# Performance work log

Hardware: AMD Instinct MI355X
Metric: run time of the kernel (lower is better)

The kernel has to match this reference:

```python
import jax, jax.numpy as jnp
import numpy as np

SCALE_FACTOR = 8.0  # sqrt(head_dim=64)
GAMMA = 1.0
NEG_INF = -1e9


def setup_inputs() -> dict:
    key = jax.random.key(0)
    kq, kk, kv, km = jax.random.split(key, 4)
    B, H, S, D = 4, 16, 2048, 64
    q = jax.random.normal(kq, (B, H, S, D), dtype=jnp.float32)
    k = jax.random.normal(kk, (B, H, S, D), dtype=jnp.float32)
    v = jax.random.normal(kv, (B, H, S, D), dtype=jnp.float32)
    mask = jax.random.randint(km, (B, 1, S, S), 0, 2, dtype=jnp.int32)
    return {"q": q, "k": k, "v": v, "mask": mask}


def reference(q, k, v, mask):
    # attn = (q/scale) @ k^T, masked, softmax along last dim, scaled by gamma
    scores = jnp.einsum("bhsd,bhtd->bhst", q / SCALE_FACTOR, k)  # [B,H,S,S]
    scores = jnp.where(mask == 0, NEG_INF, scores)
    attn = jax.nn.softmax(scores, axis=-1) * GAMMA
    output = jnp.einsum("bhst,bhtd->bhsd", attn, v) + v  # AV + residual V
    return (output, attn)
```

## Files before the change

kernel.cpp:

```cpp
#include <hip/hip_runtime.h>

typedef _Float16 f16;
typedef _Float16 f16x4 __attribute__((ext_vector_type(4)));
typedef _Float16 f16x8 __attribute__((ext_vector_type(8)));
typedef float f32x16 __attribute__((ext_vector_type(16)));

#define MFMA16(a, b, c) __builtin_amdgcn_mfma_f32_32x32x16_f16((a), (b), (c), 0, 0, 0)

constexpr int B_ = 4, H_ = 16, S_ = 2048, D_ = 64, BH = 64;
constexpr int QB = 128;
constexpr int WQ = 32;
constexpr int KB = 64;
constexpr int TS = 512;
constexpr int NSPLIT = S_ / TS;
constexpr int NKT_W = TS / KB;
constexpr int NKT = S_ / KB;
constexpr size_t OUT0 = (size_t)B_ * H_ * S_ * D_;

__device__ __forceinline__ int swzb(int row, int col ) {
  int byte = (row << 7) + (col << 1);
  return byte ^ ((row & 7) << 4);
}

__device__ __forceinline__ void kload256(const float* g, int kt, int tid, float4 kr[4]) {
#pragma unroll
  for (int rep = 0; rep < 4; ++rep) {
    int idx = (rep * 256 + tid) * 4;
    kr[rep] = *(const float4*)(g + (size_t)(kt * KB + (idx >> 6)) * D_ + (idx & 63));
  }
}
__device__ __forceinline__ void kwrite256(char* KlB, int tid, const float4 kr[4]) {
#pragma unroll
  for (int rep = 0; rep < 4; ++rep) {
    int idx = (rep * 256 + tid) * 4;
    f16x4 hx = {(f16)kr[rep].x, (f16)kr[rep].y, (f16)kr[rep].z, (f16)kr[rep].w};
    *(f16x4*)(KlB + swzb(idx >> 6, idx & 63)) = hx;
  }
}
__device__ __forceinline__ void vwrite256(char* VtB, int tid, const float4 vr[4]) {
#pragma unroll
  for (int rep = 0; rep < 4; ++rep) {
    int idx = (rep * 256 + tid) * 4;
    int row = idx >> 6, col = idx & 63;
    *(f16*)(VtB + swzb(col + 0, row)) = (f16)vr[rep].x;
    *(f16*)(VtB + swzb(col + 1, row)) = (f16)vr[rep].y;
    *(f16*)(VtB + swzb(col + 2, row)) = (f16)vr[rep].z;
    *(f16*)(VtB + swzb(col + 3, row)) = (f16)vr[rep].w;
  }
}

__device__ __forceinline__ void load_qf(const float* qg, int qrow, int hi, f16x8 qf[4]) {
  const float* qr = qg + (size_t)qrow * D_;
#pragma unroll
  for (int s = 0; s < 4; ++s) {
    const int d0 = s * 16 + hi * 8;
    float4 a = *(const float4*)(qr + d0);
    float4 c = *(const float4*)(qr + d0 + 4);
    f16x8 t;
    t[0] = (f16)(a.x * 0.125f); t[1] = (f16)(a.y * 0.125f);
    t[2] = (f16)(a.z * 0.125f); t[3] = (f16)(a.w * 0.125f);
    t[4] = (f16)(c.x * 0.125f); t[5] = (f16)(c.y * 0.125f);
    t[6] = (f16)(c.z * 0.125f); t[7] = (f16)(c.w * 0.125f);
    qf[s] = t;
  }
}

__device__ __forceinline__ f32x16 qk8(const char* KlB, const f16x8 qf[4], int sub, int ln, int hi) {
  f32x16 s;
#pragma unroll
  for (int i = 0; i < 16; ++i) s[i] = 0.0f;
#pragma unroll
  for (int t = 0; t < 4; ++t) {
    f16x8 kf = *(const f16x8*)(KlB + swzb(sub * 32 + ln, t * 16 + hi * 8));
    s = MFMA16(qf[t], kf, s);
  }
  return s;
}

__global__ void zero_ws(float* __restrict__ p, int n) {
  int i = blockIdx.x * blockDim.x + threadIdx.x;
  if (i < n) p[i] = 0.0f;
}

__global__ __launch_bounds__(256, 4) void attn_rsum(
    const float* __restrict__ qg_, const float* __restrict__ kg_,
    const int* __restrict__ mg_, float* __restrict__ ws) {
  __shared__ f16 Kl[KB * D_];
  const int tid = threadIdx.x, lane = tid & 63, wid = tid >> 6;
  const int ln = lane & 31, hi = lane >> 5;
  const int bh = blockIdx.z, b = bh >> 4;
  const int qb = blockIdx.x * QB + wid * WQ;
  const int kt0 = blockIdx.y * NKT_W;
  const float* qg = qg_ + (size_t)bh * S_ * D_;
  const float* kg = kg_ + (size_t)bh * S_ * D_;
  const int* mg = mg_ + (size_t)b * S_ * S_;
  char* KlB = (char*)Kl;

  f16x8 qf[4];
  load_qf(qg, qb + ln, hi, qf);
  float rs[16];
#pragma unroll
  for (int r = 0; r < 16; ++r) rs[r] = 0.0f;

  float4 kr[4];
  kload256(kg, kt0, tid, kr);
  for (int i = 0; i < NKT_W; ++i) {
    __syncthreads();
    kwrite256(KlB, tid, kr);
    if (i + 1 < NKT_W) kload256(kg, kt0 + i + 1, tid, kr);
    __syncthreads();
#pragma unroll
    for (int sub = 0; sub < 2; ++sub) {
      const int t0 = (kt0 + i) * KB + sub * 32;
      const int* mrow = mg + (size_t)(qb + 4 * hi) * S_ + t0 + ln;
      int mk[16];
#pragma unroll
      for (int r = 0; r < 16; ++r) {
        const int qoff = (r & 3) + 8 * (r >> 2);
        mk[r] = mrow[(size_t)qoff * S_];
      }
      f32x16 sacc = qk8(KlB, qf, sub, ln, hi);
#pragma unroll
      for (int r = 0; r < 16; ++r) rs[r] += mk[r] ? __expf(sacc[r]) : 0.0f;
    }
  }
  float* wsrow = ws + (size_t)bh * S_;
#pragma unroll
  for (int r = 0; r < 16; ++r) {
    float s = rs[r];
    s += __shfl_xor(s, 16); s += __shfl_xor(s, 8); s += __shfl_xor(s, 4);
    s += __shfl_xor(s, 2); s += __shfl_xor(s, 1);
    if (ln == 0) {
      const int qoff = (r & 3) + 8 * (r >> 2);
      atomicAdd(wsrow + qb + qoff + 4 * hi, s);
    }
  }
}

__global__ __launch_bounds__(256, 4) void attn_emit(
    const float* __restrict__ qg_, const float* __restrict__ kg_,
    const int* __restrict__ mg_, const float* __restrict__ ws,
    float* __restrict__ out) {
  __shared__ f16 Kl[KB * D_];
  const int tid = threadIdx.x, lane = tid & 63, wid = tid >> 6;
  const int ln = lane & 31, hi = lane >> 5;
  const int bh = blockIdx.z, b = bh >> 4;
  const int qb = blockIdx.x * QB + wid * WQ;
  const int kt0 = blockIdx.y * NKT_W;
  const float* qg = qg_ + (size_t)bh * S_ * D_;
  const float* kg = kg_ + (size_t)bh * S_ * D_;
  const int* mg = mg_ + (size_t)b * S_ * S_;
  float* attnp = out + OUT0 + (size_t)bh * S_ * S_;
  char* KlB = (char*)Kl;

  f16x8 qf[4];
  load_qf(qg, qb + ln, hi, qf);
  const float* wsrow = ws + (size_t)bh * S_;
  float rinv[16];
#pragma unroll
  for (int r = 0; r < 16; ++r) {
    const int qoff = (r & 3) + 8 * (r >> 2);
    rinv[r] = 1.0f / wsrow[qb + qoff + 4 * hi];
  }

  float4 kr[4];
  kload256(kg, kt0, tid, kr);
  for (int i = 0; i < NKT_W; ++i) {
    __syncthreads();
    kwrite256(KlB, tid, kr);
    if (i + 1 < NKT_W) kload256(kg, kt0 + i + 1, tid, kr);
    __syncthreads();
#pragma unroll
    for (int sub = 0; sub < 2; ++sub) {
      const int t0 = (kt0 + i) * KB + sub * 32;
      const int* mrow = mg + (size_t)(qb + 4 * hi) * S_ + t0 + ln;
      int mk[16];
#pragma unroll
      for (int r = 0; r < 16; ++r) {
        const int qoff = (r & 3) + 8 * (r >> 2);
        mk[r] = mrow[(size_t)qoff * S_];
      }
      f32x16 sacc = qk8(KlB, qf, sub, ln, hi);
      float* arow = attnp + (size_t)(qb + 4 * hi) * S_ + t0 + ln;
#pragma unroll
      for (int r = 0; r < 16; ++r) {
        const int qoff = (r & 3) + 8 * (r >> 2);
        float p = mk[r] ? __expf(sacc[r]) * rinv[r] : 0.0f;
        arow[(size_t)qoff * S_] = p;
      }
    }
  }
}

__global__ __launch_bounds__(256) void attn_out(
    const float* __restrict__ qg_, const float* __restrict__ kg_,
    const float* __restrict__ vg_, const int* __restrict__ mg_,
    const float* __restrict__ ws, float* __restrict__ out) {
  __shared__ f16 Kl[KB * D_];
  __shared__ f16 Vt[D_ * KB];
  __shared__ f16 Pl[4 * WQ * KB];
  const int tid = threadIdx.x, lane = tid & 63, wid = tid >> 6;
  const int ln = lane & 31, hi = lane >> 5;
  const int bh = blockIdx.y, b = bh >> 4;
  const int qb = blockIdx.x * QB + wid * WQ;
  const float* qg = qg_ + (size_t)bh * S_ * D_;
  const float* kg = kg_ + (size_t)bh * S_ * D_;
  const float* vg = vg_ + (size_t)bh * S_ * D_;
  const int* mg = mg_ + (size_t)b * S_ * S_;
  float* outp = out + (size_t)bh * S_ * D_;
  char* KlB = (char*)Kl;
  char* VtB = (char*)Vt;
  char* PlB = (char*)Pl + wid * (WQ * KB * 2);

  f16x8 qf[4];
  load_qf(qg, qb + ln, hi, qf);
  const float* wsrow = ws + (size_t)bh * S_;
  float rinv[16];
#pragma unroll
  for (int r = 0; r < 16; ++r) {
    const int qoff = (r & 3) + 8 * (r >> 2);
    rinv[r] = 1.0f / wsrow[qb + qoff + 4 * hi];
  }

  f32x16 oacc0, oacc1;
#pragma unroll
  for (int i = 0; i < 16; ++i) { oacc0[i] = 0.0f; oacc1[i] = 0.0f; }

  float4 kr[4], vr[4];
  kload256(kg, 0, tid, kr);
  kload256(vg, 0, tid, vr);
  for (int kt = 0; kt < NKT; ++kt) {
    __syncthreads();
    kwrite256(KlB, tid, kr);
    vwrite256(VtB, tid, vr);
    if (kt + 1 < NKT) {
      kload256(kg, kt + 1, tid, kr);
      kload256(vg, kt + 1, tid, vr);
    }
    __syncthreads();
#pragma unroll
    for (int sub = 0; sub < 2; ++sub) {
      const int t0 = kt * KB + sub * 32;
      const int* mrow = mg + (size_t)(qb + 4 * hi) * S_ + t0 + ln;
      int mk[16];
#pragma unroll
      for (int r = 0; r < 16; ++r) {
        const int qoff = (r & 3) + 8 * (r >> 2);
        mk[r] = mrow[(size_t)qoff * S_];
      }
      f32x16 sacc = qk8(KlB, qf, sub, ln, hi);
#pragma unroll
      for (int r = 0; r < 16; ++r) {
        const int qoff = (r & 3) + 8 * (r >> 2);
        float p = mk[r] ? __expf(sacc[r]) * rinv[r] : 0.0f;
        *(f16*)(PlB + swzb(qoff + 4 * hi, sub * 32 + ln)) = (f16)p;
      }
    }
#pragma unroll
    for (int ts = 0; ts < 4; ++ts) {
      f16x8 pa = *(const f16x8*)(PlB + swzb(ln, ts * 16 + hi * 8));
      f16x8 vb0 = *(const f16x8*)(VtB + swzb(ln, ts * 16 + hi * 8));
      f16x8 vb1 = *(const f16x8*)(VtB + swzb(32 + ln, ts * 16 + hi * 8));
      oacc0 = MFMA16(pa, vb0, oacc0);
      oacc1 = MFMA16(pa, vb1, oacc1);
    }
  }

#pragma unroll
  for (int r = 0; r < 16; ++r) {
    const int qoff = (r & 3) + 8 * (r >> 2);
    const size_t o = (size_t)(qb + qoff + 4 * hi) * D_ + ln;
    outp[o] = oacc0[r] + vg[o];
    outp[o + 32] = oacc1[r] + vg[o + 32];
  }
}

extern "C" void kernel_launch(void* const* d_in, const int* in_sizes, int n_in,
                              void* d_out, int out_size, void* d_ws, size_t ws_size,
                              hipStream_t stream) {
  (void)in_sizes; (void)n_in; (void)out_size; (void)ws_size;
  const float* q = (const float*)d_in[0];
  const float* k = (const float*)d_in[1];
  const float* v = (const float*)d_in[2];
  const int* mask = (const int*)d_in[3];
  float* out = (float*)d_out;
  float* wsf = (float*)d_ws;

  const int nsum = BH * S_;
  zero_ws<<<dim3((nsum + 255) / 256), dim3(256), 0, stream>>>(wsf, nsum);
  attn_rsum<<<dim3(S_ / QB, NSPLIT, BH), dim3(256), 0, stream>>>(q, k, mask, wsf);
  attn_emit<<<dim3(S_ / QB, NSPLIT, BH), dim3(256), 0, stream>>>(q, k, mask, wsf, out);
  attn_out<<<dim3(S_ / QB, BH), dim3(256), 0, stream>>>(q, k, v, mask, wsf, out);
}
```

Measured before the change: 2.154 ms.

## Pack int32 mask into bitmask and remap block order across XCDs

Adds a pre-pass that turns the int32 mask into a bitmask with one bit per element, using wavefront ballots. All three attention kernels then read one 32-bit word per row per 32 keys instead of 32 ints, cutting the mask traffic that each of the three passes repeats. The grids are also flattened to 1D and block indices remapped, (i&7)*N + (i>>3), so that consecutive work items land on the same XCD and share cache. The cost is an extra kernel launch and workspace for the packed mask.

```diff
diff --git a/kernel.cpp b/kernel.cpp
--- a/kernel.cpp
+++ b/kernel.cpp
@@ -15,7 +15,9 @@
 constexpr int NSPLIT = S_ / TS;
 constexpr int NKT_W = TS / KB;
 constexpr int NKT = S_ / KB;
+constexpr int MW = S_ / 32;
 constexpr size_t OUT0 = (size_t)B_ * H_ * S_ * D_;
+constexpr size_t WS_RSUM_OFF = (size_t)B_ * S_ * MW;
 
 __device__ __forceinline__ int swzb(int row, int col ) {
   int byte = (row << 7) + (col << 1);
@@ -82,18 +84,36 @@
   if (i < n) p[i] = 0.0f;
 }
 
+__global__ __launch_bounds__(256) void mask_pack(const int* __restrict__ mg,
+                                                 unsigned* __restrict__ mb) {
+  const int tid = threadIdx.x, lane = tid & 63, wid = tid >> 6;
+  const int row = blockIdx.x * 4 + wid;
+  const int* mrow = mg + (size_t)row * S_;
+  unsigned long long myw = 0;
+#pragma unroll
+  for (int w = 0; w < 32; ++w) {
+    int m = mrow[w * 64 + lane];
+    unsigned long long bal = __ballot(m != 0);
+    if (lane == w) myw = bal;
+  }
+  if (lane < 32) *(unsigned long long*)(mb + (size_t)row * MW + 2 * lane) = myw;
+}
+
 __global__ __launch_bounds__(256, 4) void attn_rsum(
     const float* __restrict__ qg_, const float* __restrict__ kg_,
-    const int* __restrict__ mg_, float* __restrict__ ws) {
+    const unsigned* __restrict__ mb, float* __restrict__ ws) {
   __shared__ f16 Kl[KB * D_];
   const int tid = threadIdx.x, lane = tid & 63, wid = tid >> 6;
   const int ln = lane & 31, hi = lane >> 5;
-  const int bh = blockIdx.z, b = bh >> 4;
-  const int qb = blockIdx.x * QB + wid * WQ;
-  const int kt0 = blockIdx.y * NKT_W;
+  const int i = blockIdx.x;
+  const int work = (i & 7) * 512 + (i >> 3);
+  const int bh = work >> 6, rem = work & 63;
+  const int qb = (rem & 15) * QB + wid * WQ;
+  const int kt0 = (rem >> 4) * NKT_W;
+  const int b = bh >> 4;
   const float* qg = qg_ + (size_t)bh * S_ * D_;
   const float* kg = kg_ + (size_t)bh * S_ * D_;
-  const int* mg = mg_ + (size_t)b * S_ * S_;
+  const unsigned* mbB = mb + (size_t)b * S_ * MW;
   char* KlB = (char*)Kl;
 
   f16x8 qf[4];
@@ -104,24 +124,21 @@
 
   float4 kr[4];
   kload256(kg, kt0, tid, kr);
-  for (int i = 0; i < NKT_W; ++i) {
+  for (int it = 0; it < NKT_W; ++it) {
     __syncthreads();
     kwrite256(KlB, tid, kr);
-    if (i + 1 < NKT_W) kload256(kg, kt0 + i + 1, tid, kr);
+    if (it + 1 < NKT_W) kload256(kg, kt0 + it + 1, tid, kr);
     __syncthreads();
 #pragma unroll
     for (int sub = 0; sub < 2; ++sub) {
-      const int t0 = (kt0 + i) * KB + sub * 32;
-      const int* mrow = mg + (size_t)(qb + 4 * hi) * S_ + t0 + ln;
-      int mk[16];
+      const int t0 = (kt0 + it) * KB + sub * 32;
+      f32x16 sacc = qk8(KlB, qf, sub, ln, hi);
 #pragma unroll
       for (int r = 0; r < 16; ++r) {
         const int qoff = (r & 3) + 8 * (r >> 2);
-        mk[r] = mrow[(size_t)qoff * S_];
+        const unsigned mw = mbB[(size_t)(qb + qoff + 4 * hi) * MW + (t0 >> 5)];
+        rs[r] += ((mw >> ln) & 1u) ? __expf(sacc[r]) : 0.0f;
       }
-      f32x16 sacc = qk8(KlB, qf, sub, ln, hi);
-#pragma unroll
-      for (int r = 0; r < 16; ++r) rs[r] += mk[r] ? __expf(sacc[r]) : 0.0f;
     }
   }
   float* wsrow = ws + (size_t)bh * S_;
@@ -139,17 +156,20 @@
 
 __global__ __launch_bounds__(256, 4) void attn_emit(
     const float* __restrict__ qg_, const float* __restrict__ kg_,
-    const int* __restrict__ mg_, const float* __restrict__ ws,
+    const unsigned* __restrict__ mb, const float* __restrict__ ws,
     float* __restrict__ out) {
   __shared__ f16 Kl[KB * D_];
   const int tid = threadIdx.x, lane = tid & 63, wid = tid >> 6;
   const int ln = lane & 31, hi = lane >> 5;
-  const int bh = blockIdx.z, b = bh >> 4;
-  const int qb = blockIdx.x * QB + wid * WQ;
-  const int kt0 = blockIdx.y * NKT_W;
+  const int i = blockIdx.x;
+  const int work = (i & 7) * 512 + (i >> 3);
+  const int bh = work >> 6, rem = work & 63;
+  const int qb = (rem & 15) * QB + wid * WQ;
+  const int kt0 = (rem >> 4) * NKT_W;
+  const int b = bh >> 4;
   const float* qg = qg_ + (size_t)bh * S_ * D_;
   const float* kg = kg_ + (size_t)bh * S_ * D_;
-  const int* mg = mg_ + (size_t)b * S_ * S_;
+  const unsigned* mbB = mb + (size_t)b * S_ * MW;
   float* attnp = out + OUT0 + (size_t)bh * S_ * S_;
   char* KlB = (char*)Kl;
 
@@ -165,27 +185,21 @@
 
   float4 kr[4];
   kload256(kg, kt0, tid, kr);
-  for (int i = 0; i < NKT_W; ++i) {
+  for (int it = 0; it < NKT_W; ++it) {
     __syncthreads();
     kwrite256(KlB, tid, kr);
-    if (i + 1 < NKT_W) kload256(kg, kt0 + i + 1, tid, kr);
+    if (it + 1 < NKT_W) kload256(kg, kt0 + it + 1, tid, kr);
     __syncthreads();
 #pragma unroll
     for (int sub = 0; sub < 2; ++sub) {
-      const int t0 = (kt0 + i) * KB + sub * 32;
-      const int* mrow = mg + (size_t)(qb + 4 * hi) * S_ + t0 + ln;
-      int mk[16];
+      const int t0 = (kt0 + it) * KB + sub * 32;
+      f32x16 sacc = qk8(KlB, qf, sub, ln, hi);
+      float* arow = attnp + (size_t)(qb + 4 * hi) * S_ + t0 + ln;
 #pragma unroll
       for (int r = 0; r < 16; ++r) {
         const int qoff = (r & 3) + 8 * (r >> 2);
-        mk[r] = mrow[(size_t)qoff * S_];
-      }
-      f32x16 sacc = qk8(KlB, qf, sub, ln, hi);
-      float* arow = attnp + (size_t)(qb + 4 * hi) * S_ + t0 + ln;
-#pragma unroll
-      for (int r = 0; r < 16; ++r) {
-        const int qoff = (r & 3) + 8 * (r >> 2);
-        float p = mk[r] ? __expf(sacc[r]) * rinv[r] : 0.0f;
+        const unsigned mw = mbB[(size_t)(qb + qoff + 4 * hi) * MW + (t0 >> 5)];
+        float p = ((mw >> ln) & 1u) ? __expf(sacc[r]) * rinv[r] : 0.0f;
         arow[(size_t)qoff * S_] = p;
       }
     }
@@ -194,19 +208,22 @@
 
 __global__ __launch_bounds__(256) void attn_out(
     const float* __restrict__ qg_, const float* __restrict__ kg_,
-    const float* __restrict__ vg_, const int* __restrict__ mg_,
+    const float* __restrict__ vg_, const unsigned* __restrict__ mb,
     const float* __restrict__ ws, float* __restrict__ out) {
   __shared__ f16 Kl[KB * D_];
   __shared__ f16 Vt[D_ * KB];
   __shared__ f16 Pl[4 * WQ * KB];
   const int tid = threadIdx.x, lane = tid & 63, wid = tid >> 6;
   const int ln = lane & 31, hi = lane >> 5;
-  const int bh = blockIdx.y, b = bh >> 4;
-  const int qb = blockIdx.x * QB + wid * WQ;
+  const int i = blockIdx.x;
+  const int work = (i & 7) * 128 + (i >> 3);
+  const int bh = work >> 4;
+  const int qb = (work & 15) * QB + wid * WQ;
+  const int b = bh >> 4;
   const float* qg = qg_ + (size_t)bh * S_ * D_;
   const float* kg = kg_ + (size_t)bh * S_ * D_;
   const float* vg = vg_ + (size_t)bh * S_ * D_;
-  const int* mg = mg_ + (size_t)b * S_ * S_;
+  const unsigned* mbB = mb + (size_t)b * S_ * MW;
   float* outp = out + (size_t)bh * S_ * D_;
   char* KlB = (char*)Kl;
   char* VtB = (char*)Vt;
@@ -224,7 +241,7 @@
 
   f32x16 oacc0, oacc1;
 #pragma unroll
-  for (int i = 0; i < 16; ++i) { oacc0[i] = 0.0f; oacc1[i] = 0.0f; }
+  for (int i2 = 0; i2 < 16; ++i2) { oacc0[i2] = 0.0f; oacc1[i2] = 0.0f; }
 
   float4 kr[4], vr[4];
   kload256(kg, 0, tid, kr);
@@ -241,18 +258,12 @@
 #pragma unroll
     for (int sub = 0; sub < 2; ++sub) {
       const int t0 = kt * KB + sub * 32;
-      const int* mrow = mg + (size_t)(qb + 4 * hi) * S_ + t0 + ln;
-      int mk[16];
+      f32x16 sacc = qk8(KlB, qf, sub, ln, hi);
 #pragma unroll
       for (int r = 0; r < 16; ++r) {
         const int qoff = (r & 3) + 8 * (r >> 2);
-        mk[r] = mrow[(size_t)qoff * S_];
-      }
-      f32x16 sacc = qk8(KlB, qf, sub, ln, hi);
-#pragma unroll
-      for (int r = 0; r < 16; ++r) {
-        const int qoff = (r & 3) + 8 * (r >> 2);
-        float p = mk[r] ? __expf(sacc[r]) * rinv[r] : 0.0f;
+        const unsigned mw = mbB[(size_t)(qb + qoff + 4 * hi) * MW + (t0 >> 5)];
+        float p = ((mw >> ln) & 1u) ? __expf(sacc[r]) * rinv[r] : 0.0f;
         *(f16*)(PlB + swzb(qoff + 4 * hi, sub * 32 + ln)) = (f16)p;
       }
     }
@@ -284,11 +295,13 @@
   const float* v = (const float*)d_in[2];
   const int* mask = (const int*)d_in[3];
   float* out = (float*)d_out;
-  float* wsf = (float*)d_ws;
+  unsigned* mb = (unsigned*)d_ws;
+  float* rs = (float*)d_ws + WS_RSUM_OFF;
 
   const int nsum = BH * S_;
-  zero_ws<<<dim3((nsum + 255) / 256), dim3(256), 0, stream>>>(wsf, nsum);
-  attn_rsum<<<dim3(S_ / QB, NSPLIT, BH), dim3(256), 0, stream>>>(q, k, mask, wsf);
-  attn_emit<<<dim3(S_ / QB, NSPLIT, BH), dim3(256), 0, stream>>>(q, k, mask, wsf, out);
-  attn_out<<<dim3(S_ / QB, BH), dim3(256), 0, stream>>>(q, k, v, mask, wsf, out);
-}
+  zero_ws<<<dim3((nsum + 255) / 256), dim3(256), 0, stream>>>(rs, nsum);
+  mask_pack<<<dim3(B_ * S_ / 4), dim3(256), 0, stream>>>(mask, mb);
+  attn_rsum<<<dim3(16 * NSPLIT * BH), dim3(256), 0, stream>>>(q, k, mb, rs);
+  attn_emit<<<dim3(16 * NSPLIT * BH), dim3(256), 0, stream>>>(q, k, mb, rs, out);
+  attn_out<<<dim3(16 * BH), dim3(256), 0, stream>>>(q, k, v, mb, rs, out);
+}
```

Measured after the change: 1.937 ms. 1.11x faster.
